# Kernel tuning notes

Hardware: AMD Instinct MI355X
Metric: run time of the kernel (lower is better)

The kernel has to match this reference:

```python
import jax, jax.numpy as jnp
import numpy as np

DIM = 2048          # args.dim
E = 16              # n_routed_experts
TOPK = 2            # n_activated_experts
H = 1408            # moe_inter_dim (expert hidden)
N_SHARED = 2        # n_shared_experts
HS = H * N_SHARED   # shared expert hidden
B, S = 2, 2048
TEMP = 1.0          # gate_temperature


def setup_inputs() -> dict:
    key = jax.random.key(0)
    ks = jax.random.split(key, 8)
    sc = 0.02
    return {
        "x": jax.random.normal(ks[0], (B, S, DIM), dtype=jnp.float32),
        "gate_w": jax.random.normal(ks[1], (E, DIM), dtype=jnp.float32) * sc,
        "w1": jax.random.normal(ks[2], (E, H, DIM), dtype=jnp.float32) * sc,
        "w2": jax.random.normal(ks[3], (E, DIM, H), dtype=jnp.float32) * sc,
        "w3": jax.random.normal(ks[4], (E, H, DIM), dtype=jnp.float32) * sc,
        "sw1": jax.random.normal(ks[5], (HS, DIM), dtype=jnp.float32) * sc,
        "sw2": jax.random.normal(ks[6], (DIM, HS), dtype=jnp.float32) * sc,
        "sw3": jax.random.normal(ks[7], (HS, DIM), dtype=jnp.float32) * sc,
    }


def reference(x, gate_w, w1, w2, w3, sw1, sw2, sw3):
    b, s, d = x.shape
    xf = x.reshape(-1, d)  # [T, D]

    # shared expert (SwiGLU FFN)
    sh = jax.nn.silu(xf @ sw1.T) * (xf @ sw3.T)      # [T, HS]
    shared_out = sh @ sw2.T                           # [T, D]

    # gate (eval mode: no input noise)
    scores = (xf @ gate_w.T) / TEMP                   # [T, E]
    probs = jax.nn.softmax(scores, axis=-1)
    topk_vals, topk_idx = jax.lax.top_k(probs, TOPK)  # sorted desc, matches torch.topk
    topk_vals = topk_vals / (topk_vals.sum(-1, keepdims=True) + 1e-9)

    # combine weights per (token, expert); zero where expert not selected
    w = (jax.nn.one_hot(topk_idx, E, dtype=xf.dtype) * topk_vals[..., None]).sum(1)  # [T, E]

    # all-expert SwiGLU, weighted-combined (w==0 exactly zeroes unselected experts)
    h1 = jnp.einsum('td,ehd->teh', xf, w1)            # [T, E, H]
    h3 = jnp.einsum('td,ehd->teh', xf, w3)
    act = jax.nn.silu(h1) * h3 * w[:, :, None]
    y = jnp.einsum('teh,edh->td', act, w2) + shared_out

    # aux load-balancing loss
    importance = probs.mean(0)                        # [E]
    load = w.sum(0) / (w.sum() + 1e-9)                # [E]
    aux_loss = E * (importance * load).sum()

    return y.reshape(b, s, d), aux_loss
```

## Files before the change

kernel.cpp:

```cpp
#include <hip/hip_runtime.h>
#include <cstdint>

#define TOKS 4096
#define DIMD 2048
#define NE   16
#define HE   1408
#define HSH  2816
#define SLOTS 8192
#define SLOTP 8320
#define MAXTILES 128

typedef unsigned short u16;
typedef __attribute__((ext_vector_type(8))) __bf16 bf16x8;
typedef __attribute__((ext_vector_type(4))) float  f32x4;

__device__ inline unsigned f2bf_pack(float a, float b) {
  unsigned ua = __builtin_bit_cast(unsigned, a);
  unsigned ub = __builtin_bit_cast(unsigned, b);
  ua = (ua + 0x7FFFu + ((ua >> 16) & 1u)) >> 16;
  ub = (ub + 0x7FFFu + ((ub >> 16) & 1u)) >> 16;
  return ua | (ub << 16);
}
__device__ inline u16 f2bf(float a) {
  unsigned ua = __builtin_bit_cast(unsigned, a);
  return (u16)((ua + 0x7FFFu + ((ua >> 16) & 1u)) >> 16);
}
__device__ inline float bf2f(u16 u) {
  return __builtin_bit_cast(float, (unsigned)u << 16);
}
__device__ inline void gload_lds16(const u16* g, u16* l) {
  __builtin_amdgcn_global_load_lds((const __attribute__((address_space(1))) void*)g,
                                   (__attribute__((address_space(3))) void*)l, 16, 0, 0);
}

__global__ __launch_bounds__(64)
void gate2_kernel(const float* __restrict__ x, const float* __restrict__ gw,
                  float* __restrict__ probs, int* __restrict__ sel0, int* __restrict__ sel1,
                  float* __restrict__ wt0, float* __restrict__ wt1)
{
  const int t = blockIdx.x;
  const int l = threadIdx.x;
  const float4* xr = (const float4*)(x + (size_t)t * DIMD);
  float4 xv[8];
#pragma unroll
  for (int j = 0; j < 8; ++j) xv[j] = xr[j * 64 + l];

  float sc[16];
#pragma unroll
  for (int e = 0; e < 16; ++e) {
    const float4* g = (const float4*)(gw + (size_t)e * DIMD);
    float s = 0.f;
#pragma unroll
    for (int j = 0; j < 8; ++j) {
      float4 gv = g[j * 64 + l];
      s += xv[j].x * gv.x + xv[j].y * gv.y + xv[j].z * gv.z + xv[j].w * gv.w;
    }
#pragma unroll
    for (int o = 32; o > 0; o >>= 1) s += __shfl_down(s, o);
    sc[e] = s;
  }
  if (l == 0) {
    float mx = sc[0];
#pragma unroll
    for (int e = 1; e < 16; ++e) mx = fmaxf(mx, sc[e]);
    float pe[16]; float sum = 0.f;
#pragma unroll
    for (int e = 0; e < 16; ++e) { pe[e] = __expf(sc[e] - mx); sum += pe[e]; }
    float inv = 1.f / sum;
    int b0 = -1, b1 = -1; float v0 = -1.f, v1 = -1.f;
#pragma unroll
    for (int e = 0; e < 16; ++e) {
      float p = pe[e] * inv;
      probs[t * 16 + e] = p;
      if (p > v0) { v1 = v0; b1 = b0; v0 = p; b0 = e; }
      else if (p > v1) { v1 = p; b1 = e; }
    }
    float wsum = v0 + v1 + 1e-9f;
    sel0[t] = b0; sel1[t] = b1;
    wt0[t] = v0 / wsum; wt1[t] = v1 / wsum;
  }
}

__global__ __launch_bounds__(256)
void expert_count(const int* __restrict__ sel0, const int* __restrict__ sel1,
                  const float* __restrict__ wt0, const float* __restrict__ wt1,
                  int* __restrict__ counts, float* __restrict__ loadsum)
{
  const int e = blockIdx.x, tid = threadIdx.x;
  int c = 0; float s = 0.f;
  for (int t = tid; t < TOKS; t += 256) {
    if (sel0[t] == e) { c++; s += wt0[t]; }
    else if (sel1[t] == e) { c++; s += wt1[t]; }
  }
  __shared__ int ci[256]; __shared__ float sf[256];
  ci[tid] = c; sf[tid] = s; __syncthreads();
  for (int d = 128; d > 0; d >>= 1) {
    if (tid < d) { ci[tid] += ci[tid + d]; sf[tid] += sf[tid + d]; }
    __syncthreads();
  }
  if (tid == 0) { counts[e] = ci[0]; loadsum[e] = sf[0]; }
}

__global__ __launch_bounds__(256)
void offsets_aux(const float* __restrict__ probs, const int* __restrict__ counts,
                 const float* __restrict__ loadsum, int* __restrict__ offs,
                 int* __restrict__ tile_e, int* __restrict__ tile_m, int* __restrict__ meta,
                 float* __restrict__ out_aux)
{
  const int tid = threadIdx.x;
  float imp[16];
#pragma unroll
  for (int e = 0; e < 16; ++e) imp[e] = 0.f;
  for (int t = tid; t < TOKS; t += 256)
#pragma unroll
    for (int e = 0; e < 16; ++e) imp[e] += probs[t * 16 + e];

  __shared__ float red[256];
  __shared__ float impE[16];
  for (int e = 0; e < 16; ++e) {
    red[tid] = imp[e]; __syncthreads();
    for (int d = 128; d > 0; d >>= 1) {
      if (tid < d) red[tid] += red[tid + d];
      __syncthreads();
    }
    if (tid == 0) impE[e] = red[0];
    __syncthreads();
  }
  if (tid == 0) {
    int off = 0;
    for (int e = 0; e < 16; ++e) { offs[e] = off; off += counts[e]; }
    float tot = 0.f;
    for (int e = 0; e < 16; ++e) tot += loadsum[e];
    float aux = 0.f;
    for (int e = 0; e < 16; ++e) aux += (impE[e] / (float)TOKS) * (loadsum[e] / (tot + 1e-9f));
    *out_aux = 16.f * aux;
    int tile = 0;
    for (int e = 0; e < 16; ++e) {
      int nt = (counts[e] + 255) >> 8;
      for (int k = 0; k < nt; ++k) { tile_e[tile] = e; tile_m[tile] = k << 8; ++tile; }
    }
    meta[0] = tile;
  }
}

__global__ __launch_bounds__(256)
void rank_scatter(const int* __restrict__ sel0, const int* __restrict__ sel1,
                  const float* __restrict__ wt0, const float* __restrict__ wt1,
                  const int* __restrict__ offs, int* __restrict__ toklist2,
                  float* __restrict__ slotwt, int* __restrict__ tokslot)
{
  const int e = blockIdx.x, tid = threadIdx.x;
  const int t0 = tid * 16;
  unsigned flags = 0; int cloc = 0;
#pragma unroll
  for (int j = 0; j < 16; ++j) {
    int t = t0 + j;
    bool f = (sel0[t] == e) || (sel1[t] == e);
    flags |= ((unsigned)f) << j;
    cloc += f;
  }
  __shared__ int psum[256];
  psum[tid] = cloc; __syncthreads();
  for (int d = 1; d < 256; d <<= 1) {
    int v = (tid >= d) ? psum[tid - d] : 0;
    __syncthreads();
    psum[tid] += v;
    __syncthreads();
  }
  int r = offs[e] + psum[tid] - cloc;
  for (int j = 0; j < 16; ++j) {
    if ((flags >> j) & 1u) {
      int t = t0 + j;
      bool first = (sel0[t] == e);
      toklist2[r] = t;
      slotwt[r] = first ? wt0[t] : wt1[t];
      tokslot[2 * t + (first ? 0 : 1)] = r;
      r++;
    }
  }
}

__global__ __launch_bounds__(256)
void cvt_f32_bf16(const float4* __restrict__ src, uint2* __restrict__ dst, int n4)
{
  int i = blockIdx.x * 256 + threadIdx.x;
  int stride = gridDim.x * 256;
  for (; i < n4; i += stride) {
    float4 v = src[i];
    uint2 p; p.x = f2bf_pack(v.x, v.y); p.y = f2bf_pack(v.z, v.w);
    dst[i] = p;
  }
}

__global__ __launch_bounds__(256)
void cvt_expert(const float4* __restrict__ src, uint2* __restrict__ dst,
                int per_e4, int dstride4, int doff4, int total4)
{
  int i = blockIdx.x * 256 + threadIdx.x;
  int stride = gridDim.x * 256;
  for (; i < total4; i += stride) {
    int e = i / per_e4;
    int r = i - e * per_e4;
    float4 v = src[i];
    uint2 p; p.x = f2bf_pack(v.x, v.y); p.y = f2bf_pack(v.z, v.w);
    dst[(size_t)e * dstride4 + doff4 + r] = p;
  }
}

__global__ __launch_bounds__(256)
void gather2(const float* __restrict__ x, const int* __restrict__ toklist2,
             u16* __restrict__ Xg)
{
  int slot = blockIdx.x * 4 + (threadIdx.x >> 6);
  int l = threadIdx.x & 63;
  int tok = toklist2[slot];
  const float4* srcr = (const float4*)(x + (size_t)tok * DIMD);
  uint2* dstr = (uint2*)(Xg + (size_t)slot * DIMD);
#pragma unroll
  for (int j = 0; j < 8; ++j) {
    float4 v = srcr[j * 64 + l];
    uint2 q; q.x = f2bf_pack(v.x, v.y); q.y = f2bf_pack(v.z, v.w);
    dstr[j * 64 + l] = q;
  }
}

template<int MODE, int BMT>
__global__ __launch_bounds__(512, 2)
void gemm256(const u16* __restrict__ A, const u16* __restrict__ Bg,
             u16* __restrict__ Obf, float* __restrict__ Of,
             const int* __restrict__ counts, const int* __restrict__ offs,
             const int* __restrict__ tile_e, const int* __restrict__ tile_m,
             const int* __restrict__ meta)
{
  constexpr int KD = (MODE == 0) ? DIMD : (MODE == 1) ? HSH : (MODE == 2) ? DIMD : HE;
  constexpr int ND = (MODE == 0) ? 2 * HSH : (MODE == 1) ? DIMD : (MODE == 2) ? HSH : DIMD;
  constexpr int BM = BMT * 32;
  constexpr int NT = KD / 64;

  __shared__ u16 sA[2][BM * 64];
  __shared__ u16 sB[2][256 * 64];

  const int tid  = threadIdx.x;
  const int lane = tid & 63;
  const int wave = tid >> 6;
  const int wm = wave >> 2;
  const int wn = wave & 3;

  int mbase, nbase;
  int e = 0, cnt = 0, arow0;
  const u16* B = Bg;
  if constexpr (MODE >= 2) {
    int tix = blockIdx.y;
    if (tix >= meta[0]) return;
    e = tile_e[tix];
    cnt = counts[e];
    mbase = tile_m[tix];
    arow0 = offs[e] + mbase;
    nbase = blockIdx.x * 256;
    B = Bg + (size_t)e * ND * KD;
  } else {
    const int nx = gridDim.x;
    int nwg = nx * gridDim.y;
    int bid = blockIdx.y * nx + blockIdx.x;
    int q = nwg >> 3, r2 = nwg & 7;
    int xcd = bid & 7, pos = bid >> 3;
    int wgid = (xcd < r2 ? xcd * (q + 1) : r2 * (q + 1) + (xcd - r2) * q) + pos;
    mbase = (wgid / nx) * BM;
    nbase = (wgid % nx) * 256;
    arow0 = mbase;
  }

  f32x4 acc[BMT][4];
#pragma unroll
  for (int i = 0; i < BMT; ++i)
#pragma unroll
    for (int j = 0; j < 4; ++j) acc[i][j] = (f32x4){0.f, 0.f, 0.f, 0.f};

  const int srow = lane >> 3;
  const int scol = ((lane & 7) ^ srow) * 8;
  const u16* Bbase = B + (size_t)nbase * KD;

  const u16* Asrc[BMT / 2];
#pragma unroll
  for (int i = 0; i < BMT / 2; ++i) {
    int c = wave * (BMT / 2) + i;
    int row = c * 8 + srow;
    int rg = arow0 + row;
    if constexpr (MODE >= 2) { if (rg > SLOTS - 1) rg = SLOTS - 1; }
    Asrc[i] = A + (size_t)rg * KD + scol;
  }
  const u16* Bsrc[4];
#pragma unroll
  for (int i = 0; i < 4; ++i) {
    int c = wave * 4 + i;
    Bsrc[i] = Bbase + (size_t)(c * 8 + srow) * KD + scol;
  }

#define STAGE_T(bb, kb) do {                                                    \
    _Pragma("unroll") for (int i_ = 0; i_ < BMT / 2; ++i_)                      \
      gload_lds16(Asrc[i_] + (kb), &sA[bb][(wave * (BMT / 2) + i_) * 512]);     \
    _Pragma("unroll") for (int i_ = 0; i_ < 4; ++i_)                            \
      gload_lds16(Bsrc[i_] + (kb), &sB[bb][(wave * 4 + i_) * 512]);             \
  } while (0)

  const int lm = lane & 15, hi = lane >> 4;
  int aoff0[BMT], boff0[4];
#pragma unroll
  for (int mi = 0; mi < BMT; ++mi) {
    int r = wm * (BMT * 16) + mi * 16 + lm;
    aoff0[mi] = r * 128 + ((hi ^ (r & 7)) << 4);
  }
#pragma unroll
  for (int ni = 0; ni < 4; ++ni) {
    int r = wn * 64 + ni * 16 + lm;
    boff0[ni] = r * 128 + ((hi ^ (r & 7)) << 4);
  }

  STAGE_T(0, 0);
  STAGE_T(1, 64);
  int cur = 0;
  for (int t = 0; t < NT; ++t) {
    if (t < NT - 1) {
      if constexpr (BMT == 8) asm volatile("s_waitcnt vmcnt(8)" ::: "memory");
      else                    asm volatile("s_waitcnt vmcnt(6)" ::: "memory");
    } else {
      asm volatile("s_waitcnt vmcnt(0)" ::: "memory");
    }
    __builtin_amdgcn_s_barrier();
    __builtin_amdgcn_sched_barrier(0);

    const char* sAc = (const char*)&sA[cur][0];
    const char* sBc = (const char*)&sB[cur][0];
    __builtin_amdgcn_s_setprio(1);
#pragma unroll
    for (int ks = 0; ks < 2; ++ks) {
      const int kx = ks << 6;
      bf16x8 b[4];
#pragma unroll
      for (int ni = 0; ni < 4; ++ni) b[ni] = *(const bf16x8*)(sBc + (boff0[ni] ^ kx));
#pragma unroll
      for (int mi = 0; mi < BMT; ++mi) {
        bf16x8 av = *(const bf16x8*)(sAc + (aoff0[mi] ^ kx));
#pragma unroll
        for (int ni = 0; ni < 4; ++ni)
          acc[mi][ni] = __builtin_amdgcn_mfma_f32_16x16x32_bf16(av, b[ni], acc[mi][ni], 0, 0, 0);
      }
    }
    __builtin_amdgcn_s_setprio(0);
    __builtin_amdgcn_sched_barrier(0);
    __builtin_amdgcn_s_barrier();
    __builtin_amdgcn_sched_barrier(0);
    if (t + 2 < NT) STAGE_T(cur, (t + 2) * 64);
    cur ^= 1;
  }
#undef STAGE_T

  const int lr4 = hi * 4;
#pragma unroll
  for (int mi = 0; mi < BMT; ++mi) {
#pragma unroll
    for (int ni = 0; ni < 4; ++ni) {
#pragma unroll
      for (int r = 0; r < 4; ++r) {
        int lrow = wm * (BMT * 16) + mi * 16 + lr4 + r;
        int col  = nbase + wn * 64 + ni * 16 + lm;
        float v = acc[mi][ni][r];
        if constexpr (MODE == 0) {
          Obf[(size_t)(mbase + lrow) * ND + col] = f2bf(v);
        } else if constexpr (MODE == 1) {
          Of[(size_t)(mbase + lrow) * ND + col] = v;
        } else {
          int grow = mbase + lrow;
          if (grow < cnt) Obf[(size_t)(arow0 + lrow) * ND + col] = f2bf(v);
        }
      }
    }
  }
}

__global__ __launch_bounds__(256)
void combine_sh(const u16* __restrict__ H, u16* __restrict__ U)
{
  int i = blockIdx.x * 256 + threadIdx.x;
  if (i >= TOKS * (HSH / 8)) return;
  int t = i / (HSH / 8);
  int c = (i - t * (HSH / 8)) * 8;
  const u16* h1p = H + (size_t)t * (2 * HSH) + c;
  uint4 va = *(const uint4*)h1p;
  uint4 vb = *(const uint4*)(h1p + HSH);
  const u16* ap = (const u16*)&va;
  const u16* bp = (const u16*)&vb;
  u16 o[8];
#pragma unroll
  for (int j = 0; j < 8; ++j) {
    float v1 = bf2f(ap[j]), v3 = bf2f(bp[j]);
    o[j] = f2bf((v1 / (1.f + __expf(-v1))) * v3);
  }
  *(uint4*)(U + (size_t)t * HSH + c) = *(const uint4*)o;
}

__global__ __launch_bounds__(256)
void combine_r(const u16* __restrict__ H, const float* __restrict__ slotwt,
               u16* __restrict__ Act)
{
  int i = blockIdx.x * 256 + threadIdx.x;
  if (i >= SLOTS * (HE / 8)) return;
  int t = i / (HE / 8);
  int c = (i - t * (HE / 8)) * 8;
  float wt = slotwt[t];
  const u16* h1p = H + (size_t)t * HSH + c;
  uint4 va = *(const uint4*)h1p;
  uint4 vb = *(const uint4*)(h1p + HE);
  const u16* ap = (const u16*)&va;
  const u16* bp = (const u16*)&vb;
  u16 o[8];
#pragma unroll
  for (int j = 0; j < 8; ++j) {
    float v1 = bf2f(ap[j]), v3 = bf2f(bp[j]);
    o[j] = f2bf((v1 / (1.f + __expf(-v1))) * v3 * wt);
  }
  *(uint4*)(Act + (size_t)t * HE + c) = *(const uint4*)o;
}

__global__ __launch_bounds__(256)
void finalize(const u16* __restrict__ Yslot, const int* __restrict__ tokslot,
              float* __restrict__ out)
{
  int i = blockIdx.x * 256 + threadIdx.x;
  int t = i >> 8;
  int c = (i & 255) * 8;
  int s0 = tokslot[2 * t], s1 = tokslot[2 * t + 1];
  uint4 a = *(const uint4*)(Yslot + (size_t)s0 * DIMD + c);
  uint4 b = *(const uint4*)(Yslot + (size_t)s1 * DIMD + c);
  const u16* ap = (const u16*)&a;
  const u16* bp = (const u16*)&b;
  float* op = out + (size_t)t * DIMD + c;
  float4 v0 = *(float4*)op, v1 = *(float4*)(op + 4);
  float vv[8] = {v0.x, v0.y, v0.z, v0.w, v1.x, v1.y, v1.z, v1.w};
#pragma unroll
  for (int j = 0; j < 8; ++j) vv[j] += bf2f(ap[j]) + bf2f(bp[j]);
  *(float4*)op = (float4){vv[0], vv[1], vv[2], vv[3]};
  *(float4*)(op + 4) = (float4){vv[4], vv[5], vv[6], vv[7]};
}

extern "C" void kernel_launch(void* const* d_in, const int* in_sizes, int n_in,
                              void* d_out, int out_size, void* d_ws, size_t ws_size,
                              hipStream_t stream) {
  const float* x      = (const float*)d_in[0];
  const float* gate_w = (const float*)d_in[1];
  const float* w1     = (const float*)d_in[2];
  const float* w2     = (const float*)d_in[3];
  const float* w3     = (const float*)d_in[4];
  const float* sw1    = (const float*)d_in[5];
  const float* sw2    = (const float*)d_in[6];
  const float* sw3    = (const float*)d_in[7];
  float* out = (float*)d_out;

  char* ws = (char*)d_ws;
  size_t o = 0;
  int*   counts   = (int*)(ws + o);   o += 256;
  int*   offsv    = (int*)(ws + o);   o += 256;
  float* loadsum  = (float*)(ws + o); o += 256;
  int*   tile_e   = (int*)(ws + o);   o += MAXTILES * 4;
  int*   tile_m   = (int*)(ws + o);   o += MAXTILES * 4;
  int*   meta     = (int*)(ws + o);   o += 256;
  int*   sel0     = (int*)(ws + o);   o += TOKS * 4;
  int*   sel1     = (int*)(ws + o);   o += TOKS * 4;
  float* wt0      = (float*)(ws + o); o += TOKS * 4;
  float* wt1      = (float*)(ws + o); o += TOKS * 4;
  int*   tokslot  = (int*)(ws + o);   o += TOKS * 2 * 4;
  int*   toklist2 = (int*)(ws + o);   o += SLOTS * 4;
  float* slotwt   = (float*)(ws + o); o += SLOTS * 4;
  float* probs    = (float*)(ws + o); o += TOKS * 16 * 4;

  o = 1 << 20;
  u16* xbf   = (u16*)(ws + o); o += (size_t)TOKS * DIMD * 2;
  u16* Xg    = (u16*)(ws + o); o += (size_t)SLOTP * DIMD * 2;
  u16* w13b  = (u16*)(ws + o); o += (size_t)NE * HSH * DIMD * 2;
  u16* w2b   = (u16*)(ws + o); o += (size_t)NE * DIMD * HE * 2;
  u16* sw13b = (u16*)(ws + o); o += (size_t)(2 * HSH) * DIMD * 2;
  u16* sw2b  = (u16*)(ws + o); o += (size_t)DIMD * HSH * 2;
  u16* H     = (u16*)(ws + o); o += (size_t)SLOTP * HSH * 2;
  u16* UA    = (u16*)(ws + o); o += (size_t)SLOTP * HE * 2;
  u16* Yslot = Xg;

  gate2_kernel<<<TOKS, 64, 0, stream>>>(x, gate_w, probs, sel0, sel1, wt0, wt1);
  expert_count<<<NE, 256, 0, stream>>>(sel0, sel1, wt0, wt1, counts, loadsum);
  offsets_aux<<<1, 256, 0, stream>>>(probs, counts, loadsum, offsv, tile_e, tile_m, meta,
                                     out + (size_t)TOKS * DIMD);
  rank_scatter<<<NE, 256, 0, stream>>>(sel0, sel1, wt0, wt1, offsv, toklist2, slotwt, tokslot);

  cvt_f32_bf16<<<2048, 256, 0, stream>>>((const float4*)x, (uint2*)xbf, TOKS * DIMD / 4);
  cvt_f32_bf16<<<1024, 256, 0, stream>>>((const float4*)sw1, (uint2*)sw13b, HSH * DIMD / 4);
  cvt_f32_bf16<<<1024, 256, 0, stream>>>((const float4*)sw3, (uint2*)sw13b + HSH * DIMD / 4, HSH * DIMD / 4);
  cvt_f32_bf16<<<1024, 256, 0, stream>>>((const float4*)sw2, (uint2*)sw2b, DIMD * HSH / 4);
  cvt_f32_bf16<<<4096, 256, 0, stream>>>((const float4*)w2, (uint2*)w2b, NE * DIMD * HE / 4);
  cvt_expert<<<4096, 256, 0, stream>>>((const float4*)w1, (uint2*)w13b,
                                       HE * DIMD / 4, HSH * DIMD / 4, 0, NE * HE * DIMD / 4);
  cvt_expert<<<4096, 256, 0, stream>>>((const float4*)w3, (uint2*)w13b,
                                       HE * DIMD / 4, HSH * DIMD / 4, HE * DIMD / 4, NE * HE * DIMD / 4);
  gather2<<<SLOTS / 4, 256, 0, stream>>>(x, toklist2, Xg);

  gemm256<0, 8><<<dim3(2 * HSH / 256, TOKS / 256), 512, 0, stream>>>(
      xbf, sw13b, H, nullptr, nullptr, nullptr, nullptr, nullptr, nullptr);
  combine_sh<<<TOKS * (HSH / 8) / 256, 256, 0, stream>>>(H, UA);
  gemm256<1, 4><<<dim3(DIMD / 256, TOKS / 128), 512, 0, stream>>>(
      UA, sw2b, nullptr, out, nullptr, nullptr, nullptr, nullptr, nullptr);

  gemm256<2, 8><<<dim3(HSH / 256, 48), 512, 0, stream>>>(
      Xg, w13b, H, nullptr, counts, offsv, tile_e, tile_m, meta);
  combine_r<<<SLOTS * (HE / 8) / 256, 256, 0, stream>>>(H, slotwt, UA);
  gemm256<3, 8><<<dim3(DIMD / 256, 48), 512, 0, stream>>>(
      UA, w2b, Yslot, nullptr, counts, offsv, tile_e, tile_m, meta);
  finalize<<<TOKS * DIMD / 8 / 256, 256, 0, stream>>>(Yslot, tokslot, out);
}
```

Before: 841.6 us.

## Restructure GEMM main loop into an 8-phase interleaved LDS pipeline; use 128-row tiles for down-projection

Rewrites the bf16 GEMM inner loop so each K-tile is split into half-K sub-buffers. Global-to-LDS loads for the next stages are issued between MFMA phase groups, and partial vmcnt waits plus barriers replace a single wait per tile, so memory traffic overlaps compute more finely. It also uses a new LDS swizzle and adds a second routed-tile list with 128-row tiles, which the expert down-projection GEMM now uses (BMT 4, more blocks) to reduce padding waste and raise occupancy. The cost is more barriers per tile, tricky vmcnt accounting that could race if miscounted, and more scheduling bookkeeping.

```diff
diff --git a/kernel.cpp b/kernel.cpp
--- a/kernel.cpp
+++ b/kernel.cpp
@@ -31,6 +31,9 @@
 __device__ inline void gload_lds16(const u16* g, u16* l) {
   __builtin_amdgcn_global_load_lds((const __attribute__((address_space(1))) void*)g,
                                    (__attribute__((address_space(3))) void*)l, 16, 0, 0);
+}
+template<int N> __device__ __attribute__((always_inline)) inline void vmwait() {
+  if constexpr (N >= 0) asm volatile("s_waitcnt vmcnt(%0)" :: "i"(N) : "memory");
 }
 
 __global__ __launch_bounds__(64)
@@ -104,7 +107,8 @@
 __global__ __launch_bounds__(256)
 void offsets_aux(const float* __restrict__ probs, const int* __restrict__ counts,
                  const float* __restrict__ loadsum, int* __restrict__ offs,
-                 int* __restrict__ tile_e, int* __restrict__ tile_m, int* __restrict__ meta,
+                 int* __restrict__ te256, int* __restrict__ tm256, int* __restrict__ me256,
+                 int* __restrict__ te128, int* __restrict__ tm128, int* __restrict__ me128,
                  float* __restrict__ out_aux)
 {
   const int tid = threadIdx.x;
@@ -134,12 +138,14 @@
     float aux = 0.f;
     for (int e = 0; e < 16; ++e) aux += (impE[e] / (float)TOKS) * (loadsum[e] / (tot + 1e-9f));
     *out_aux = 16.f * aux;
-    int tile = 0;
+    int t2 = 0, t1 = 0;
     for (int e = 0; e < 16; ++e) {
-      int nt = (counts[e] + 255) >> 8;
-      for (int k = 0; k < nt; ++k) { tile_e[tile] = e; tile_m[tile] = k << 8; ++tile; }
+      int n2 = (counts[e] + 255) >> 8;
+      for (int k = 0; k < n2; ++k) { te256[t2] = e; tm256[t2] = k << 8; ++t2; }
+      int n1 = (counts[e] + 127) >> 7;
+      for (int k = 0; k < n1; ++k) { te128[t1] = e; tm128[t1] = k << 7; ++t1; }
     }
-    meta[0] = tile;
+    me256[0] = t2; me128[0] = t1;
   }
 }
 
@@ -226,19 +232,22 @@
 
 template<int MODE, int BMT>
 __global__ __launch_bounds__(512, 2)
-void gemm256(const u16* __restrict__ A, const u16* __restrict__ Bg,
-             u16* __restrict__ Obf, float* __restrict__ Of,
-             const int* __restrict__ counts, const int* __restrict__ offs,
-             const int* __restrict__ tile_e, const int* __restrict__ tile_m,
-             const int* __restrict__ meta)
+void gemm8p(const u16* __restrict__ A, const u16* __restrict__ Bg,
+            u16* __restrict__ Obf, float* __restrict__ Of,
+            const int* __restrict__ counts, const int* __restrict__ offs,
+            const int* __restrict__ tile_e, const int* __restrict__ tile_m,
+            const int* __restrict__ meta)
 {
   constexpr int KD = (MODE == 0) ? DIMD : (MODE == 1) ? HSH : (MODE == 2) ? DIMD : HE;
   constexpr int ND = (MODE == 0) ? 2 * HSH : (MODE == 1) ? DIMD : (MODE == 2) ? HSH : DIMD;
   constexpr int BM = BMT * 32;
   constexpr int NT = KD / 64;
-
-  __shared__ u16 sA[2][BM * 64];
-  __shared__ u16 sB[2][256 * 64];
+  constexpr int ARNDS = BM / 128;
+  constexpr int VMS = (BMT == 8) ? 8 : 6;
+  constexpr int VMP = (BMT == 8) ? 4 : 3;
+
+  __shared__ u16 sA[2 * 2 * BM * 32];
+  __shared__ u16 sB[2 * 2 * 256 * 32];
 
   const int tid  = threadIdx.x;
   const int lane = tid & 63;
@@ -276,93 +285,110 @@
 #pragma unroll
     for (int j = 0; j < 4; ++j) acc[i][j] = (f32x4){0.f, 0.f, 0.f, 0.f};
 
-  const int srow = lane >> 3;
-  const int scol = ((lane & 7) ^ srow) * 8;
-  const u16* Bbase = B + (size_t)nbase * KD;
-
-  const u16* Asrc[BMT / 2];
-#pragma unroll
-  for (int i = 0; i < BMT / 2; ++i) {
-    int c = wave * (BMT / 2) + i;
-    int row = c * 8 + srow;
-    int rg = arow0 + row;
-    if constexpr (MODE >= 2) { if (rg > SLOTS - 1) rg = SLOTS - 1; }
-    Asrc[i] = A + (size_t)rg * KD + scol;
-  }
-  const u16* Bsrc[4];
-#pragma unroll
-  for (int i = 0; i < 4; ++i) {
-    int c = wave * 4 + i;
-    Bsrc[i] = Bbase + (size_t)(c * 8 + srow) * KD + scol;
-  }
-
-#define STAGE_T(bb, kb) do {                                                    \
-    _Pragma("unroll") for (int i_ = 0; i_ < BMT / 2; ++i_)                      \
-      gload_lds16(Asrc[i_] + (kb), &sA[bb][(wave * (BMT / 2) + i_) * 512]);     \
-    _Pragma("unroll") for (int i_ = 0; i_ < 4; ++i_)                            \
-      gload_lds16(Bsrc[i_] + (kb), &sB[bb][(wave * 4 + i_) * 512]);             \
+  const int r4 = tid >> 2, c4 = tid & 3;
+  const u16* Aptr[ARNDS];
+#pragma unroll
+  for (int r = 0; r < ARNDS; ++r) {
+    int row = r * 128 + r4;
+    int grow = arow0 + row;
+    if constexpr (MODE >= 2) { if (grow > SLOTS - 1) grow = SLOTS - 1; }
+    int slot = c4 ^ ((row >> 1) & 3);
+    Aptr[r] = A + (size_t)grow * KD + slot * 8;
+  }
+  const u16* Bptr[2];
+#pragma unroll
+  for (int r = 0; r < 2; ++r) {
+    int row = r * 128 + r4;
+    int slot = c4 ^ ((row >> 1) & 3);
+    Bptr[r] = B + (size_t)(nbase + row) * KD + slot * 8;
+  }
+
+  const char* sAc = (const char*)sA;
+  const char* sBc = (const char*)sB;
+  const int lm = lane & 15, hi = lane >> 4;
+
+#define STAGE_A(b, kt, ks) { _Pragma("unroll") for (int r_ = 0; r_ < ARNDS; ++r_) \
+    gload_lds16(Aptr[r_] + (kt) * 64 + (ks) * 32, \
+                sA + (((b) * 2 + (ks)) * BM + r_ * 128 + wave * 16) * 32); }
+#define STAGE_B(b, kt, ks) { _Pragma("unroll") for (int r_ = 0; r_ < 2; ++r_) \
+    gload_lds16(Bptr[r_] + (kt) * 64 + (ks) * 32, \
+                sB + (((b) * 2 + (ks)) * 256 + r_ * 128 + wave * 16) * 32); }
+#define LDB_ALL(ks, b) { _Pragma("unroll") for (int n_ = 0; n_ < 4; ++n_) { \
+    int r_ = wn * 64 + n_ * 16 + lm; \
+    bfr[n_] = *(const bf16x8*)(sBc + (((b) * 2 + (ks)) * 256 + r_) * 64 + ((hi ^ ((r_ >> 1) & 3)) << 4)); } }
+#define LDA_G(mg, ks, b) { _Pragma("unroll") for (int i_ = 0; i_ < BMT / 2; ++i_) { \
+    int r_ = wm * (BMT * 16) + ((mg) * (BMT / 2) + i_) * 16 + lm; \
+    afr[i_] = *(const bf16x8*)(sAc + (((b) * 2 + (ks)) * BM + r_) * 64 + ((hi ^ ((r_ >> 1) & 3)) << 4)); } }
+#define MFMA_G(mg) { _Pragma("unroll") for (int i_ = 0; i_ < BMT / 2; ++i_) { \
+    bf16x8 av_ = afr[i_]; \
+    _Pragma("unroll") for (int n_ = 0; n_ < 4; ++n_) \
+      acc[(mg) * (BMT / 2) + i_][n_] = \
+        __builtin_amdgcn_mfma_f32_16x16x32_bf16(av_, bfr[n_], acc[(mg) * (BMT / 2) + i_][n_], 0, 0, 0); } }
+#define PHASE_TAIL() \
+    __builtin_amdgcn_s_barrier(); \
+    asm volatile("s_waitcnt lgkmcnt(0)" ::: "memory"); \
+    __builtin_amdgcn_sched_barrier(0); \
+    __builtin_amdgcn_s_setprio(1);
+#define PHASE_END() \
+    __builtin_amdgcn_s_setprio(0); \
+    __builtin_amdgcn_sched_barrier(0);
+
+#define KTILE(ktv, DO01, DO23, VM1N, VM3N) do { \
+    const int b_ = (ktv) & 1; \
+    bf16x8 afr[BMT / 2]; \
+     \
+    LDB_ALL(0, b_); \
+    LDA_G(0, 0, b_); \
+    if (DO01) STAGE_A(b_ ^ 1, (ktv) + 1, 1); \
+    PHASE_TAIL(); MFMA_G(0); PHASE_END(); \
+    __builtin_amdgcn_s_barrier(); \
+     \
+    LDA_G(1, 0, b_); \
+    if (DO01) STAGE_B(b_ ^ 1, (ktv) + 1, 1); \
+    PHASE_TAIL(); MFMA_G(1); PHASE_END(); \
+    vmwait<VM1N>(); \
+    __builtin_amdgcn_s_barrier(); \
+     \
+    LDB_ALL(1, b_); \
+    LDA_G(0, 1, b_); \
+    if (DO23) STAGE_A(b_, (ktv) + 2, 0); \
+    PHASE_TAIL(); MFMA_G(0); PHASE_END(); \
+    __builtin_amdgcn_s_barrier(); \
+     \
+    LDA_G(1, 1, b_); \
+    if (DO23) STAGE_B(b_, (ktv) + 2, 0); \
+    PHASE_TAIL(); MFMA_G(1); PHASE_END(); \
+    vmwait<VM3N>(); \
+    __builtin_amdgcn_s_barrier(); \
   } while (0)
 
-  const int lm = lane & 15, hi = lane >> 4;
-  int aoff0[BMT], boff0[4];
+  STAGE_A(0, 0, 0); STAGE_B(0, 0, 0);
+  STAGE_A(0, 0, 1); STAGE_B(0, 0, 1);
+  STAGE_A(1, 1, 0); STAGE_B(1, 1, 0);
+  vmwait<VMS>();
+  __builtin_amdgcn_s_barrier();
+
+  bf16x8 bfr[4];
+  for (int t = 0; t < NT - 2; ++t) KTILE(t, true, true, VMS, VMS);
+  KTILE(NT - 2, true, false, VMS, VMP);
+  KTILE(NT - 1, false, false, 0, -1);
+
+#undef KTILE
+#undef PHASE_END
+#undef PHASE_TAIL
+#undef MFMA_G
+#undef LDA_G
+#undef LDB_ALL
+#undef STAGE_B
+#undef STAGE_A
+
 #pragma unroll
   for (int mi = 0; mi < BMT; ++mi) {
-    int r = wm * (BMT * 16) + mi * 16 + lm;
-    aoff0[mi] = r * 128 + ((hi ^ (r & 7)) << 4);
-  }
-#pragma unroll
-  for (int ni = 0; ni < 4; ++ni) {
-    int r = wn * 64 + ni * 16 + lm;
-    boff0[ni] = r * 128 + ((hi ^ (r & 7)) << 4);
-  }
-
-  STAGE_T(0, 0);
-  STAGE_T(1, 64);
-  int cur = 0;
-  for (int t = 0; t < NT; ++t) {
-    if (t < NT - 1) {
-      if constexpr (BMT == 8) asm volatile("s_waitcnt vmcnt(8)" ::: "memory");
-      else                    asm volatile("s_waitcnt vmcnt(6)" ::: "memory");
-    } else {
-      asm volatile("s_waitcnt vmcnt(0)" ::: "memory");
-    }
-    __builtin_amdgcn_s_barrier();
-    __builtin_amdgcn_sched_barrier(0);
-
-    const char* sAc = (const char*)&sA[cur][0];
-    const char* sBc = (const char*)&sB[cur][0];
-    __builtin_amdgcn_s_setprio(1);
-#pragma unroll
-    for (int ks = 0; ks < 2; ++ks) {
-      const int kx = ks << 6;
-      bf16x8 b[4];
-#pragma unroll
-      for (int ni = 0; ni < 4; ++ni) b[ni] = *(const bf16x8*)(sBc + (boff0[ni] ^ kx));
-#pragma unroll
-      for (int mi = 0; mi < BMT; ++mi) {
-        bf16x8 av = *(const bf16x8*)(sAc + (aoff0[mi] ^ kx));
-#pragma unroll
-        for (int ni = 0; ni < 4; ++ni)
-          acc[mi][ni] = __builtin_amdgcn_mfma_f32_16x16x32_bf16(av, b[ni], acc[mi][ni], 0, 0, 0);
-      }
-    }
-    __builtin_amdgcn_s_setprio(0);
-    __builtin_amdgcn_sched_barrier(0);
-    __builtin_amdgcn_s_barrier();
-    __builtin_amdgcn_sched_barrier(0);
-    if (t + 2 < NT) STAGE_T(cur, (t + 2) * 64);
-    cur ^= 1;
-  }
-#undef STAGE_T
-
-  const int lr4 = hi * 4;
-#pragma unroll
-  for (int mi = 0; mi < BMT; ++mi) {
 #pragma unroll
     for (int ni = 0; ni < 4; ++ni) {
 #pragma unroll
       for (int r = 0; r < 4; ++r) {
-        int lrow = wm * (BMT * 16) + mi * 16 + lr4 + r;
+        int lrow = wm * (BMT * 16) + mi * 16 + hi * 4 + r;
         int col  = nbase + wn * 64 + ni * 16 + lm;
         float v = acc[mi][ni][r];
         if constexpr (MODE == 0) {
@@ -461,9 +487,12 @@
   int*   counts   = (int*)(ws + o);   o += 256;
   int*   offsv    = (int*)(ws + o);   o += 256;
   float* loadsum  = (float*)(ws + o); o += 256;
-  int*   tile_e   = (int*)(ws + o);   o += MAXTILES * 4;
-  int*   tile_m   = (int*)(ws + o);   o += MAXTILES * 4;
-  int*   meta     = (int*)(ws + o);   o += 256;
+  int*   te256    = (int*)(ws + o);   o += MAXTILES * 4;
+  int*   tm256    = (int*)(ws + o);   o += MAXTILES * 4;
+  int*   me256    = (int*)(ws + o);   o += 256;
+  int*   te128    = (int*)(ws + o);   o += MAXTILES * 4;
+  int*   tm128    = (int*)(ws + o);   o += MAXTILES * 4;
+  int*   me128    = (int*)(ws + o);   o += 256;
   int*   sel0     = (int*)(ws + o);   o += TOKS * 4;
   int*   sel1     = (int*)(ws + o);   o += TOKS * 4;
   float* wt0      = (float*)(ws + o); o += TOKS * 4;
@@ -486,7 +515,8 @@
 
   gate2_kernel<<<TOKS, 64, 0, stream>>>(x, gate_w, probs, sel0, sel1, wt0, wt1);
   expert_count<<<NE, 256, 0, stream>>>(sel0, sel1, wt0, wt1, counts, loadsum);
-  offsets_aux<<<1, 256, 0, stream>>>(probs, counts, loadsum, offsv, tile_e, tile_m, meta,
+  offsets_aux<<<1, 256, 0, stream>>>(probs, counts, loadsum, offsv,
+                                     te256, tm256, me256, te128, tm128, me128,
                                      out + (size_t)TOKS * DIMD);
   rank_scatter<<<NE, 256, 0, stream>>>(sel0, sel1, wt0, wt1, offsv, toklist2, slotwt, tokslot);
 
@@ -501,16 +531,16 @@
                                        HE * DIMD / 4, HSH * DIMD / 4, HE * DIMD / 4, NE * HE * DIMD / 4);
   gather2<<<SLOTS / 4, 256, 0, stream>>>(x, toklist2, Xg);
 
-  gemm256<0, 8><<<dim3(2 * HSH / 256, TOKS / 256), 512, 0, stream>>>(
+  gemm8p<0, 8><<<dim3(2 * HSH / 256, TOKS / 256), 512, 0, stream>>>(
       xbf, sw13b, H, nullptr, nullptr, nullptr, nullptr, nullptr, nullptr);
   combine_sh<<<TOKS * (HSH / 8) / 256, 256, 0, stream>>>(H, UA);
-  gemm256<1, 4><<<dim3(DIMD / 256, TOKS / 128), 512, 0, stream>>>(
+  gemm8p<1, 4><<<dim3(DIMD / 256, TOKS / 128), 512, 0, stream>>>(
       UA, sw2b, nullptr, out, nullptr, nullptr, nullptr, nullptr, nullptr);
 
-  gemm256<2, 8><<<dim3(HSH / 256, 48), 512, 0, stream>>>(
-      Xg, w13b, H, nullptr, counts, offsv, tile_e, tile_m, meta);
+  gemm8p<2, 8><<<dim3(HSH / 256, 48), 512, 0, stream>>>(
+      Xg, w13b, H, nullptr, counts, offsv, te256, tm256, me256);
   combine_r<<<SLOTS * (HE / 8) / 256, 256, 0, stream>>>(H, slotwt, UA);
-  gemm256<3, 8><<<dim3(DIMD / 256, 48), 512, 0, stream>>>(
-      UA, w2b, Yslot, nullptr, counts, offsv, tile_e, tile_m, meta);
+  gemm8p<3, 4><<<dim3(DIMD / 256, 80), 512, 0, stream>>>(
+      UA, w2b, Yslot, nullptr, counts, offsv, te128, tm128, me128);
   finalize<<<TOKS * DIMD / 8 / 256, 256, 0, stream>>>(Yslot, tokslot, out);
 }
```

New measurement: 910.2 us. 1.08x slower.
